# Performance work log

Measured on AMD Instinct MI355X. Metric: run time of the kernel, lower is better.

The kernel has to match this reference:

```python
import jax, jax.numpy as jnp
import numpy as np
import math

B, L, D, P = 2, 2048, 256, 32

def _lin_init(key, fan_in, shape):
    return jax.random.normal(key, shape, dtype=jnp.float32) / np.float32(math.sqrt(fan_in))

def setup_inputs() -> dict:
    key = jax.random.key(0)
    ks = jax.random.split(key, 16)
    return {
        "x": jax.random.normal(ks[0], (B, L, D), dtype=jnp.float32),
        "pos_phases": jax.random.normal(ks[1], (L, P), dtype=jnp.float32) * np.float32(math.pi),
        "w_pos_value": _lin_init(ks[2], D, (D, D)), "b_pos_value": jnp.zeros((D,), jnp.float32),
        "w_key": _lin_init(ks[3], D, (D, P)), "b_key": jnp.zeros((P,), jnp.float32),
        "w_kv": _lin_init(ks[4], D, (D, D)), "b_kv": jnp.zeros((D,), jnp.float32),
        "w_vg1": _lin_init(ks[5], 2 * D, (2 * D, D)), "b_vg1": jnp.zeros((D,), jnp.float32),
        "w_vg2": _lin_init(ks[6], D, (D, 1)), "b_vg2": jnp.zeros((1,), jnp.float32),
        "w_bg1": _lin_init(ks[7], D, (D, D // 2)), "b_bg1": jnp.zeros((D // 2,), jnp.float32),
        "w_bg2": _lin_init(ks[8], D // 2, (D // 2, 2)), "b_bg2": jnp.zeros((2,), jnp.float32),
        "ln_r_g": jnp.ones((D,), jnp.float32), "ln_r_b": jnp.zeros((D,), jnp.float32),
        "w_r1": _lin_init(ks[9], D, (D, 2 * D)), "b_r1": jnp.zeros((2 * D,), jnp.float32),
        "w_r2": _lin_init(ks[10], 2 * D, (2 * D, D)), "b_r2": jnp.zeros((D,), jnp.float32),
        "ln_o_g": jnp.ones((D,), jnp.float32), "ln_o_b": jnp.zeros((D,), jnp.float32),
        "w_out": _lin_init(ks[11], D, (D, D)), "b_out": jnp.zeros((D,), jnp.float32),
    }

def _ln(z, g, b, eps=1e-5):
    mu = z.mean(-1, keepdims=True)
    var = ((z - mu) ** 2).mean(-1, keepdims=True)
    return (z - mu) * jax.lax.rsqrt(var + eps) * g + b

def _shift1(z):
    # torch.roll(shifts=1, dims=1) then zero first position == shift right with zero pad
    return jnp.concatenate([jnp.zeros_like(z[:, :1]), z[:, :-1]], axis=1)

def reference(x, pos_phases, w_pos_value, b_pos_value, w_key, b_key, w_kv, b_kv,
              w_vg1, b_vg1, w_vg2, b_vg2, w_bg1, b_bg1, w_bg2, b_bg2,
              ln_r_g, ln_r_b, w_r1, b_r1, w_r2, b_r2, ln_o_g, ln_o_b, w_out, b_out):
    Bv, Lv, Dv = x.shape
    Pv = pos_phases.shape[1]
    inv_sqrt_p = np.float32(1.0 / math.sqrt(Pv))

    # --- positional memory ---
    pos_phasors = jnp.exp(1j * pos_phases)                      # (L,P) complex64
    pos_values = (x @ w_pos_value + b_pos_value).astype(jnp.complex64)  # (B,L,D)
    pos_bound = pos_phasors[None, :, :, None] * pos_values[:, :, None, :]  # (B,L,P,D)
    pos_memory = jnp.cumsum(pos_bound, axis=1)
    pos_query = jnp.exp(-1j * pos_phases)                       # (L,P)
    pos_retrieved = (pos_memory * pos_query[None, :, :, None]).sum(axis=2).real * inv_sqrt_p

    # --- content-based KV memory ---
    key_phases = jnp.tanh(x @ w_key + b_key) * np.float32(math.pi)  # (B,L,P)
    key_phasors = jnp.exp(1j * key_phases)
    kv_values = (x @ w_kv + b_kv).astype(jnp.complex64)         # (B,L,D)

    x_shifted = _shift1(x)
    gate_input = jnp.concatenate([x, x_shifted], axis=-1)       # (B,L,2D)
    h = jax.nn.gelu(gate_input @ w_vg1 + b_vg1, approximate=False)
    value_gates = jax.nn.sigmoid(h @ w_vg2 + b_vg2)             # (B,L,1)

    key_phasors_shifted = _shift1(key_phasors)                  # (B,L,P)
    kv_bound = (key_phasors_shifted[..., None] * kv_values[:, :, None, :]) \
               * value_gates[:, :, :, None].astype(jnp.complex64)  # (B,L,P,D)
    kv_memory = jnp.cumsum(kv_bound, axis=1)
    gate_cumsum = jnp.maximum(jnp.cumsum(value_gates, axis=1), 1.0)  # (B,L,1)
    kv_query = jnp.exp(-1j * key_phases)                        # (B,L,P)
    kv_retrieved = (kv_memory * kv_query[..., None]).sum(axis=2).real
    kv_retrieved = kv_retrieved / (jnp.sqrt(gate_cumsum) * np.float32(math.sqrt(Pv)))

    # --- blend, refine, output ---
    bg_h = jax.nn.gelu(x @ w_bg1 + b_bg1, approximate=False)
    blend = jax.nn.softmax(bg_h @ w_bg2 + b_bg2, axis=-1)       # (B,L,2)
    blended = blend[..., 0:1] * pos_retrieved + blend[..., 1:2] * kv_retrieved

    refined = jax.nn.gelu(_ln(blended, ln_r_g, ln_r_b) @ w_r1 + b_r1, approximate=False) @ w_r2 + b_r2
    return x + (_ln(refined, ln_o_g, ln_o_b) @ w_out + b_out)
```

## Files before the change

### kernel.cpp

```cpp
#include <hip/hip_runtime.h>
#include <math.h>

#define B_ 2
#define L_ 2048
#define D_ 256
#define P_ 32
#define NC_ 32
#define CL_ 64

#define INV_SQRT_P 0.17677669529663687f
#define PI_F 3.14159265358979323846f

typedef __attribute__((ext_vector_type(8))) short bf16x8;
typedef __attribute__((ext_vector_type(4))) float f32x4;

__device__ __forceinline__ float gelu_exact(float x){
    return 0.5f * x * (1.0f + erff(x * 0.70710678118654752f));
}

__device__ __forceinline__ unsigned short f2bf(float f){
    unsigned int u = __float_as_uint(f);
    u += 0x7FFFu + ((u >> 16) & 1u);
    return (unsigned short)(u >> 16);
}

__device__ __forceinline__ float bf2f(unsigned short u){
    return __uint_as_float(((unsigned int)u) << 16);
}

__global__ __launch_bounds__(256) void k_prep(
    const float* __restrict__ pos_phases,
    const float* __restrict__ w_pv, const float* __restrict__ w_kv,
    const float* __restrict__ w_vg1, const float* __restrict__ w_bg1,
    const float* __restrict__ w_r1, const float* __restrict__ w_r2,
    const float* __restrict__ w_out, const float* __restrict__ w_key,
    unsigned short* __restrict__ wq,
    float* __restrict__ cpos, float* __restrict__ spos)
{
    int id = blockIdx.x * 256 + threadIdx.x;
    if (id < 630784){
        const float* src; int N; int local;
        if (id < 65536)       { src = w_pv;  N = 256; local = id; }
        else if (id < 131072) { src = w_kv;  N = 256; local = id - 65536; }
        else if (id < 262144) { src = w_vg1; N = 256; local = id - 131072; }
        else if (id < 294912) { src = w_bg1; N = 128; local = id - 262144; }
        else if (id < 425984) { src = w_r1;  N = 512; local = id - 294912; }
        else if (id < 557056) { src = w_r2;  N = 256; local = id - 425984; }
        else if (id < 622592) { src = w_out; N = 256; local = id - 557056; }
        else                  { src = w_key; N = 32;  local = id - 622592; }
        int j = local & 7, lane = (local >> 3) & 63, tile = local >> 9;
        int NT = N >> 4;
        int nt = tile % NT, kt = tile / NT;
        int row = kt * 32 + ((lane >> 4) << 3) + j;
        int col = nt * 16 + (lane & 15);
        wq[id] = f2bf(src[(size_t)row * N + col]);
    } else {
        int idx = id - 630784;
        float s, c;
        sincosf(pos_phases[idx], &s, &c);
        cpos[idx] = c;
        spos[idx] = s;
    }
}

__global__ __launch_bounds__(512) void k_proj(
    const float* __restrict__ x,
    const unsigned short* __restrict__ wq,
    const float* __restrict__ b_pv, const float* __restrict__ b_kv,
    const float* __restrict__ b_vg1,
    const float* __restrict__ w_vg2, const float* __restrict__ b_vg2,
    const float* __restrict__ b_bg1,
    const float* __restrict__ w_bg2, const float* __restrict__ b_bg2,
    const float* __restrict__ b_key,
    unsigned short* __restrict__ pvb, unsigned short* __restrict__ kvvb,
    float* __restrict__ ck, float* __restrict__ sk,
    float* __restrict__ vg, float* __restrict__ blend0, float* __restrict__ blend1)
{
    __shared__ float hbuf[16][257];
    __shared__ float kvbuf[16][257];
    __shared__ float bhbuf[16][129];
    __shared__ float kph[16][33];
    __shared__ float red[16][17], red2[16][17], red3[16][17];
    __shared__ float vgs[16];

    const int i = threadIdx.x;
    const int lane = i & 63, w = i >> 6;
    const int b = blockIdx.x >> 7, lt = blockIdx.x & 127, l0 = lt * 16;
    const int g = lane >> 4, c = lane & 15;

    bf16x8 xa[8], xs[8];
    {
        int row  = l0 + (lane & 15);
        int rowp = row - 1;
        const float* xr = x + (size_t)(b * L_ + row) * D_ + ((lane >> 4) << 3);
        #pragma unroll
        for (int kt = 0; kt < 8; ++kt){
            float4 a0 = *(const float4*)(xr + kt * 32);
            float4 a1 = *(const float4*)(xr + kt * 32 + 4);
            bf16x8 v;
            v[0] = (short)f2bf(a0.x); v[1] = (short)f2bf(a0.y);
            v[2] = (short)f2bf(a0.z); v[3] = (short)f2bf(a0.w);
            v[4] = (short)f2bf(a1.x); v[5] = (short)f2bf(a1.y);
            v[6] = (short)f2bf(a1.z); v[7] = (short)f2bf(a1.w);
            xa[kt] = v;
        }
        if (rowp >= 0){
            const float* xp = x + (size_t)(b * L_ + rowp) * D_ + ((lane >> 4) << 3);
            #pragma unroll
            for (int kt = 0; kt < 8; ++kt){
                float4 a0 = *(const float4*)(xp + kt * 32);
                float4 a1 = *(const float4*)(xp + kt * 32 + 4);
                bf16x8 v;
                v[0] = (short)f2bf(a0.x); v[1] = (short)f2bf(a0.y);
                v[2] = (short)f2bf(a0.z); v[3] = (short)f2bf(a0.w);
                v[4] = (short)f2bf(a1.x); v[5] = (short)f2bf(a1.y);
                v[6] = (short)f2bf(a1.z); v[7] = (short)f2bf(a1.w);
                xs[kt] = v;
            }
        } else {
            #pragma unroll
            for (int kt = 0; kt < 8; ++kt){
                bf16x8 v;
                #pragma unroll
                for (int j = 0; j < 8; ++j) v[j] = 0;
                xs[kt] = v;
            }
        }
    }

    const unsigned short* wpv  = wq;
    const unsigned short* wkv  = wq + 65536;
    const unsigned short* wvg1 = wq + 131072;
    const unsigned short* wbg1 = wq + 262144;
    const unsigned short* wkey = wq + 622592;

    for (int jb = w; jb < 58; jb += 8){
        f32x4 acc = {0.f, 0.f, 0.f, 0.f};
        if (jb < 2){
            int nt = jb;
            #pragma unroll
            for (int kt = 0; kt < 8; ++kt){
                bf16x8 bf = *(const bf16x8*)(wkey + (kt * 2 + nt) * 512 + lane * 8);
                acc = __builtin_amdgcn_mfma_f32_16x16x32_bf16(xa[kt], bf, acc, 0, 0, 0);
            }
            float bb = b_key[nt * 16 + c];
            #pragma unroll
            for (int r = 0; r < 4; ++r)
                kph[4 * g + r][nt * 16 + c] = acc[r] + bb;
        } else if (jb < 18){
            int nt = jb - 2;
            #pragma unroll
            for (int kt = 0; kt < 8; ++kt){
                bf16x8 bf = *(const bf16x8*)(wpv + (kt * 16 + nt) * 512 + lane * 8);
                acc = __builtin_amdgcn_mfma_f32_16x16x32_bf16(xa[kt], bf, acc, 0, 0, 0);
            }
            float bb = b_pv[nt * 16 + c];
            #pragma unroll
            for (int r = 0; r < 4; ++r)
                pvb[(size_t)(b * L_ + l0 + 4 * g + r) * D_ + nt * 16 + c] = f2bf(acc[r] + bb);
        } else if (jb < 34){
            int nt = jb - 18;
            #pragma unroll
            for (int kt = 0; kt < 8; ++kt){
                bf16x8 bf = *(const bf16x8*)(wkv + (kt * 16 + nt) * 512 + lane * 8);
                acc = __builtin_amdgcn_mfma_f32_16x16x32_bf16(xa[kt], bf, acc, 0, 0, 0);
            }
            float bb = b_kv[nt * 16 + c];
            #pragma unroll
            for (int r = 0; r < 4; ++r)
                kvbuf[4 * g + r][nt * 16 + c] = acc[r] + bb;
        } else if (jb < 50){
            int nt = jb - 34;
            #pragma unroll
            for (int kt = 0; kt < 8; ++kt){
                bf16x8 bf = *(const bf16x8*)(wvg1 + (kt * 16 + nt) * 512 + lane * 8);
                acc = __builtin_amdgcn_mfma_f32_16x16x32_bf16(xa[kt], bf, acc, 0, 0, 0);
            }
            #pragma unroll
            for (int kt = 8; kt < 16; ++kt){
                bf16x8 bf = *(const bf16x8*)(wvg1 + (kt * 16 + nt) * 512 + lane * 8);
                acc = __builtin_amdgcn_mfma_f32_16x16x32_bf16(xs[kt - 8], bf, acc, 0, 0, 0);
            }
            float bb = b_vg1[nt * 16 + c];
            #pragma unroll
            for (int r = 0; r < 4; ++r)
                hbuf[4 * g + r][nt * 16 + c] = gelu_exact(acc[r] + bb);
        } else {
            int nt = jb - 50;
            #pragma unroll
            for (int kt = 0; kt < 8; ++kt){
                bf16x8 bf = *(const bf16x8*)(wbg1 + (kt * 8 + nt) * 512 + lane * 8);
                acc = __builtin_amdgcn_mfma_f32_16x16x32_bf16(xa[kt], bf, acc, 0, 0, 0);
            }
            float bb = b_bg1[nt * 16 + c];
            #pragma unroll
            for (int r = 0; r < 4; ++r)
                bhbuf[4 * g + r][nt * 16 + c] = gelu_exact(acc[r] + bb);
        }
    }
    __syncthreads();

    {
        int t = i >> 5, p = i & 31;
        float a = tanhf(kph[t][p]) * PI_F;
        float s, cc;
        sincosf(a, &s, &cc);
        ck[(size_t)(b * L_ + l0 + t) * P_ + p] = cc;
        sk[(size_t)(b * L_ + l0 + t) * P_ + p] = s;
    }

    if (i < 256){
        int t = i >> 4, c2 = i & 15;
        float s = 0.f;
        #pragma unroll
        for (int m = 0; m < 16; ++m){ int dd = c2 + 16 * m; s += hbuf[t][dd] * w_vg2[dd]; }
        red[t][c2] = s;
    } else {
        int ii = i - 256;
        int t = ii >> 4, c2 = ii & 15;
        float s0 = 0.f, s1 = 0.f;
        #pragma unroll
        for (int m = 0; m < 8; ++m){
            int jj = c2 + 16 * m;
            float v = bhbuf[t][jj];
            s0 += v * w_bg2[jj * 2 + 0];
            s1 += v * w_bg2[jj * 2 + 1];
        }
        red2[t][c2] = s0; red3[t][c2] = s1;
    }
    __syncthreads();
    if (i < 16){
        float s = 0.f;
        #pragma unroll
        for (int c2 = 0; c2 < 16; ++c2) s += red[i][c2];
        s += b_vg2[0];
        float gv = 1.0f / (1.0f + expf(-s));
        vg[b * L_ + l0 + i] = gv;
        vgs[i] = gv;
    } else if (i < 32){
        int t = i - 16;
        float s0 = 0.f, s1 = 0.f;
        #pragma unroll
        for (int c2 = 0; c2 < 16; ++c2){ s0 += red2[t][c2]; s1 += red3[t][c2]; }
        s0 += b_bg2[0]; s1 += b_bg2[1];
        float mx = fmaxf(s0, s1);
        float e0 = expf(s0 - mx), e1 = expf(s1 - mx);
        float inv = 1.0f / (e0 + e1);
        blend0[b * L_ + l0 + t] = e0 * inv;
        blend1[b * L_ + l0 + t] = e1 * inv;
    }
    __syncthreads();

    {
        int d = i & 255, tg = i >> 8;
        #pragma unroll
        for (int m = 0; m < 8; ++m){
            int tok = tg * 8 + m;
            kvvb[(size_t)(b * L_ + l0 + tok) * D_ + d] = f2bf(kvbuf[tok][d] * vgs[tok]);
        }
    }
}

__global__ __launch_bounds__(256) void k_scan1(
    const float* __restrict__ cpos, const float* __restrict__ spos,
    const float* __restrict__ ck, const float* __restrict__ sk,
    const unsigned short* __restrict__ pvb, const unsigned short* __restrict__ kvvb,
    const float* __restrict__ vg,
    float* __restrict__ posSr, float* __restrict__ posSi,
    float* __restrict__ kvSr, float* __restrict__ kvSi,
    float* __restrict__ rnorm)
{
    const int z = blockIdx.z;
    const int c = blockIdx.x, b = blockIdx.y;
    const int i = threadIdx.x;
    if (z == 8){
        if (c != 0) return;
        float loc[8];
        float run = 0.f;
        #pragma unroll
        for (int m = 0; m < 8; ++m){ run += vg[b * L_ + i * 8 + m]; loc[m] = run; }
        __shared__ float part[256];
        part[i] = run;
        __syncthreads();
        for (int off = 1; off < 256; off <<= 1){
            float t = (i >= off) ? part[i - off] : 0.0f;
            __syncthreads();
            part[i] += t;
            __syncthreads();
        }
        float excl = part[i] - run;
        #pragma unroll
        for (int m = 0; m < 8; ++m){
            float gc = fmaxf(excl + loc[m], 1.0f);
            rnorm[b * L_ + i * 8 + m] = rsqrtf(gc) * INV_SQRT_P;
        }
        return;
    }
    const int type = z >> 2, pg = z & 3;
    const int d = i;
    const int p0 = pg * 8;
    float Sr[8], Si[8];
    #pragma unroll
    for (int j = 0; j < 8; ++j){ Sr[j] = 0.f; Si[j] = 0.f; }

    if (type == 0){
        for (int l = 0; l < CL_; ++l){
            int row = c * CL_ + l;
            float v = bf2f(pvb[(size_t)(b * L_ + row) * D_ + d]);
            float4 c0 = *(const float4*)(cpos + row * P_ + p0);
            float4 c1 = *(const float4*)(cpos + row * P_ + p0 + 4);
            float4 s0 = *(const float4*)(spos + row * P_ + p0);
            float4 s1 = *(const float4*)(spos + row * P_ + p0 + 4);
            Sr[0] = fmaf(c0.x, v, Sr[0]); Si[0] = fmaf(s0.x, v, Si[0]);
            Sr[1] = fmaf(c0.y, v, Sr[1]); Si[1] = fmaf(s0.y, v, Si[1]);
            Sr[2] = fmaf(c0.z, v, Sr[2]); Si[2] = fmaf(s0.z, v, Si[2]);
            Sr[3] = fmaf(c0.w, v, Sr[3]); Si[3] = fmaf(s0.w, v, Si[3]);
            Sr[4] = fmaf(c1.x, v, Sr[4]); Si[4] = fmaf(s1.x, v, Si[4]);
            Sr[5] = fmaf(c1.y, v, Sr[5]); Si[5] = fmaf(s1.y, v, Si[5]);
            Sr[6] = fmaf(c1.z, v, Sr[6]); Si[6] = fmaf(s1.z, v, Si[6]);
            Sr[7] = fmaf(c1.w, v, Sr[7]); Si[7] = fmaf(s1.w, v, Si[7]);
        }
        #pragma unroll
        for (int j = 0; j < 8; ++j){
            size_t o = (size_t)((b * NC_ + c) * P_ + p0 + j) * D_ + d;
            posSr[o] = Sr[j]; posSi[o] = Si[j];
        }
    } else {
        float pc[8], ps[8];
        int srow = c * CL_ - 1;
        if (srow >= 0){
            float4 c0 = *(const float4*)(ck + ((size_t)b * L_ + srow) * P_ + p0);
            float4 c1 = *(const float4*)(ck + ((size_t)b * L_ + srow) * P_ + p0 + 4);
            float4 s0 = *(const float4*)(sk + ((size_t)b * L_ + srow) * P_ + p0);
            float4 s1 = *(const float4*)(sk + ((size_t)b * L_ + srow) * P_ + p0 + 4);
            pc[0]=c0.x; pc[1]=c0.y; pc[2]=c0.z; pc[3]=c0.w;
            pc[4]=c1.x; pc[5]=c1.y; pc[6]=c1.z; pc[7]=c1.w;
            ps[0]=s0.x; ps[1]=s0.y; ps[2]=s0.z; ps[3]=s0.w;
            ps[4]=s1.x; ps[5]=s1.y; ps[6]=s1.z; ps[7]=s1.w;
        } else {
            #pragma unroll
            for (int j = 0; j < 8; ++j){ pc[j] = 0.f; ps[j] = 0.f; }
        }
        for (int l = 0; l < CL_; ++l){
            int row = c * CL_ + l;
            float vv = bf2f(kvvb[(size_t)(b * L_ + row) * D_ + d]);
            float4 c0 = *(const float4*)(ck + ((size_t)b * L_ + row) * P_ + p0);
            float4 c1 = *(const float4*)(ck + ((size_t)b * L_ + row) * P_ + p0 + 4);
            float4 s0 = *(const float4*)(sk + ((size_t)b * L_ + row) * P_ + p0);
            float4 s1 = *(const float4*)(sk + ((size_t)b * L_ + row) * P_ + p0 + 4);
            #pragma unroll
            for (int j = 0; j < 8; ++j){
                Sr[j] = fmaf(pc[j], vv, Sr[j]);
                Si[j] = fmaf(ps[j], vv, Si[j]);
            }
            pc[0]=c0.x; pc[1]=c0.y; pc[2]=c0.z; pc[3]=c0.w;
            pc[4]=c1.x; pc[5]=c1.y; pc[6]=c1.z; pc[7]=c1.w;
            ps[0]=s0.x; ps[1]=s0.y; ps[2]=s0.z; ps[3]=s0.w;
            ps[4]=s1.x; ps[5]=s1.y; ps[6]=s1.z; ps[7]=s1.w;
        }
        #pragma unroll
        for (int j = 0; j < 8; ++j){
            size_t o = (size_t)((b * NC_ + c) * P_ + p0 + j) * D_ + d;
            kvSr[o] = Sr[j]; kvSi[o] = Si[j];
        }
    }
}

__global__ __launch_bounds__(256) void k_prefix(
    float* __restrict__ posSr, float* __restrict__ posSi,
    float* __restrict__ kvSr, float* __restrict__ kvSi)
{
    __shared__ float4 tot_s[64][4];
    const int colLocal = threadIdx.x >> 2, seg = threadIdx.x & 3;
    const int col = blockIdx.x * 64 + colLocal;
    const int a = col >> 12;
    const int rem = col & 4095;
    const int b = rem >> 11;
    const int pd = (rem & 2047) * 4;
    float* A = (a == 0) ? posSr : (a == 1) ? posSi : (a == 2) ? kvSr : kvSi;
    float* base = A + (size_t)b * NC_ * (P_ * D_) + pd;

    float4 t[8];
    #pragma unroll
    for (int k = 0; k < 8; ++k)
        t[k] = *(const float4*)(base + (size_t)(seg * 8 + k) * (P_ * D_));
    float4 tot = {0.f, 0.f, 0.f, 0.f};
    #pragma unroll
    for (int k = 0; k < 8; ++k){
        tot.x += t[k].x; tot.y += t[k].y; tot.z += t[k].z; tot.w += t[k].w;
    }
    tot_s[colLocal][seg] = tot;
    __syncthreads();
    float4 run = {0.f, 0.f, 0.f, 0.f};
    #pragma unroll
    for (int s = 0; s < 3; ++s){
        if (s < seg){
            float4 v = tot_s[colLocal][s];
            run.x += v.x; run.y += v.y; run.z += v.z; run.w += v.w;
        }
    }
    #pragma unroll
    for (int k = 0; k < 8; ++k){
        float4 cur = t[k];
        *(float4*)(base + (size_t)(seg * 8 + k) * (P_ * D_)) = run;
        run.x += cur.x; run.y += cur.y; run.z += cur.z; run.w += cur.w;
    }
}

__global__ __launch_bounds__(256) void k_retrieve(
    const float* __restrict__ cpos, const float* __restrict__ spos,
    const float* __restrict__ ck, const float* __restrict__ sk,
    const unsigned short* __restrict__ pvb, const unsigned short* __restrict__ kvvb,
    const float* __restrict__ rnorm,
    const float* __restrict__ posSr, const float* __restrict__ posSi,
    const float* __restrict__ kvSr, const float* __restrict__ kvSi,
    unsigned short* __restrict__ posretb, unsigned short* __restrict__ kvretb)
{
    const int z = blockIdx.z;
    const int c = blockIdx.x, b = blockIdx.y;
    const int type = z >> 2, dquad = z & 3;
    const int lane = threadIdx.x & 63, wv = threadIdx.x >> 6;
    const int pg = lane >> 4, dl = lane & 15;
    const int d = dquad * 64 + wv * 16 + dl;
    const int p0 = pg * 8;

    float Sr[8], Si[8];

    if (type == 0){
        #pragma unroll
        for (int j = 0; j < 8; ++j){
            size_t o = (size_t)((b * NC_ + c) * P_ + p0 + j) * D_ + d;
            Sr[j] = posSr[o]; Si[j] = posSi[o];
        }
        for (int l = 0; l < CL_; ++l){
            int row = c * CL_ + l;
            float v = bf2f(pvb[(size_t)(b * L_ + row) * D_ + d]);
            float4 c0 = *(const float4*)(cpos + row * P_ + p0);
            float4 c1 = *(const float4*)(cpos + row * P_ + p0 + 4);
            float4 s0 = *(const float4*)(spos + row * P_ + p0);
            float4 s1 = *(const float4*)(spos + row * P_ + p0 + 4);
            float r0 = 0.f, r1 = 0.f, r2 = 0.f, r3 = 0.f;
            Sr[0] = fmaf(c0.x, v, Sr[0]); r0 = fmaf(c0.x, Sr[0], r0);
            Si[0] = fmaf(s0.x, v, Si[0]); r1 = fmaf(s0.x, Si[0], r1);
            Sr[1] = fmaf(c0.y, v, Sr[1]); r2 = fmaf(c0.y, Sr[1], r2);
            Si[1] = fmaf(s0.y, v, Si[1]); r3 = fmaf(s0.y, Si[1], r3);
            Sr[2] = fmaf(c0.z, v, Sr[2]); r0 = fmaf(c0.z, Sr[2], r0);
            Si[2] = fmaf(s0.z, v, Si[2]); r1 = fmaf(s0.z, Si[2], r1);
            Sr[3] = fmaf(c0.w, v, Sr[3]); r2 = fmaf(c0.w, Sr[3], r2);
            Si[3] = fmaf(s0.w, v, Si[3]); r3 = fmaf(s0.w, Si[3], r3);
            Sr[4] = fmaf(c1.x, v, Sr[4]); r0 = fmaf(c1.x, Sr[4], r0);
            Si[4] = fmaf(s1.x, v, Si[4]); r1 = fmaf(s1.x, Si[4], r1);
            Sr[5] = fmaf(c1.y, v, Sr[5]); r2 = fmaf(c1.y, Sr[5], r2);
            Si[5] = fmaf(s1.y, v, Si[5]); r3 = fmaf(s1.y, Si[5], r3);
            Sr[6] = fmaf(c1.z, v, Sr[6]); r0 = fmaf(c1.z, Sr[6], r0);
            Si[6] = fmaf(s1.z, v, Si[6]); r1 = fmaf(s1.z, Si[6], r1);
            Sr[7] = fmaf(c1.w, v, Sr[7]); r2 = fmaf(c1.w, Sr[7], r2);
            Si[7] = fmaf(s1.w, v, Si[7]); r3 = fmaf(s1.w, Si[7], r3);
            float r = (r0 + r1) + (r2 + r3);
            r += __shfl_xor(r, 16, 64);
            r += __shfl_xor(r, 32, 64);
            if (pg == 0)
                posretb[(size_t)(b * L_ + row) * D_ + d] = f2bf(r * INV_SQRT_P);
        }
    } else {
        #pragma unroll
        for (int j = 0; j < 8; ++j){
            size_t o = (size_t)((b * NC_ + c) * P_ + p0 + j) * D_ + d;
            Sr[j] = kvSr[o]; Si[j] = kvSi[o];
        }
        float pc[8], ps[8];
        int srow = c * CL_ - 1;
        if (srow >= 0){
            float4 c0 = *(const float4*)(ck + ((size_t)b * L_ + srow) * P_ + p0);
            float4 c1 = *(const float4*)(ck + ((size_t)b * L_ + srow) * P_ + p0 + 4);
            float4 s0 = *(const float4*)(sk + ((size_t)b * L_ + srow) * P_ + p0);
            float4 s1 = *(const float4*)(sk + ((size_t)b * L_ + srow) * P_ + p0 + 4);
            pc[0]=c0.x; pc[1]=c0.y; pc[2]=c0.z; pc[3]=c0.w;
            pc[4]=c1.x; pc[5]=c1.y; pc[6]=c1.z; pc[7]=c1.w;
            ps[0]=s0.x; ps[1]=s0.y; ps[2]=s0.z; ps[3]=s0.w;
            ps[4]=s1.x; ps[5]=s1.y; ps[6]=s1.z; ps[7]=s1.w;
        } else {
            #pragma unroll
            for (int j = 0; j < 8; ++j){ pc[j] = 0.f; ps[j] = 0.f; }
        }
        for (int l = 0; l < CL_; ++l){
            int row = c * CL_ + l;
            float vv = bf2f(kvvb[(size_t)(b * L_ + row) * D_ + d]);
            float rn = rnorm[b * L_ + row];
            float4 c0 = *(const float4*)(ck + ((size_t)b * L_ + row) * P_ + p0);
            float4 c1 = *(const float4*)(ck + ((size_t)b * L_ + row) * P_ + p0 + 4);
            float4 s0 = *(const float4*)(sk + ((size_t)b * L_ + row) * P_ + p0);
            float4 s1 = *(const float4*)(sk + ((size_t)b * L_ + row) * P_ + p0 + 4);
            float qc[8], qs[8];
            qc[0]=c0.x; qc[1]=c0.y; qc[2]=c0.z; qc[3]=c0.w;
            qc[4]=c1.x; qc[5]=c1.y; qc[6]=c1.z; qc[7]=c1.w;
            qs[0]=s0.x; qs[1]=s0.y; qs[2]=s0.z; qs[3]=s0.w;
            qs[4]=s1.x; qs[5]=s1.y; qs[6]=s1.z; qs[7]=s1.w;
            float r0 = 0.f, r1 = 0.f, r2 = 0.f, r3 = 0.f;
            #pragma unroll
            for (int j = 0; j < 8; ++j){
                Sr[j] = fmaf(pc[j], vv, Sr[j]);
                Si[j] = fmaf(ps[j], vv, Si[j]);
                if (j & 1){ r2 = fmaf(qc[j], Sr[j], r2); r3 = fmaf(qs[j], Si[j], r3); }
                else      { r0 = fmaf(qc[j], Sr[j], r0); r1 = fmaf(qs[j], Si[j], r1); }
                pc[j] = qc[j]; ps[j] = qs[j];
            }
            float r = (r0 + r1) + (r2 + r3);
            r += __shfl_xor(r, 16, 64);
            r += __shfl_xor(r, 32, 64);
            if (pg == 0)
                kvretb[(size_t)(b * L_ + row) * D_ + d] = f2bf(r * rn);
        }
    }
}

__global__ __launch_bounds__(512) void k_final(
    const float* __restrict__ x,
    const unsigned short* __restrict__ posretb, const unsigned short* __restrict__ kvretb,
    const float* __restrict__ blend0, const float* __restrict__ blend1,
    const unsigned short* __restrict__ wq,
    const float* __restrict__ ln_r_g, const float* __restrict__ ln_r_b,
    const float* __restrict__ b_r1, const float* __restrict__ b_r2,
    const float* __restrict__ ln_o_g, const float* __restrict__ ln_o_b,
    const float* __restrict__ b_out,
    float* __restrict__ out)
{
    __shared__ float zbuf[16][257];
    __shared__ __align__(16) unsigned short aA[8][512];
    __shared__ __align__(16) unsigned short aH[16][512];
    __shared__ float red[16][17], red2[16][17];
    __shared__ float mu[16], rs[16];

    const int i = threadIdx.x, lane = i & 63, w = i >> 6;
    const int b = blockIdx.x >> 7, l0 = (blockIdx.x & 127) * 16;
    const int g = lane >> 4, c = lane & 15;
    const unsigned short* wr1  = wq + 294912;
    const unsigned short* wr2  = wq + 425984;
    const unsigned short* wout = wq + 557056;

    {
        int t = i >> 5, c0 = (i & 31) * 8;
        size_t base = (size_t)(b * L_ + l0 + t) * D_ + c0;
        float w0 = blend0[b * L_ + l0 + t], w1 = blend1[b * L_ + l0 + t];
        bf16x8 pp = *(const bf16x8*)(posretb + base);
        bf16x8 kk = *(const bf16x8*)(kvretb + base);
        #pragma unroll
        for (int m = 0; m < 8; ++m)
            zbuf[t][c0 + m] = w0 * bf2f((unsigned short)pp[m])
                            + w1 * bf2f((unsigned short)kk[m]);
    }
    __syncthreads();

    if (i < 256){
        int t = i >> 4, c2 = i & 15;
        float s = 0.f, s2 = 0.f;
        #pragma unroll
        for (int m = 0; m < 16; ++m){ float v = zbuf[t][c2 + 16 * m]; s += v; s2 += v * v; }
        red[t][c2] = s; red2[t][c2] = s2;
    }
    __syncthreads();
    if (i < 16){
        float s = 0.f, s2 = 0.f;
        #pragma unroll
        for (int c2 = 0; c2 < 16; ++c2){ s += red[i][c2]; s2 += red2[i][c2]; }
        float mean = s * (1.0f / 256.0f);
        float var  = s2 * (1.0f / 256.0f) - mean * mean;
        mu[i] = mean; rs[i] = rsqrtf(var + 1e-5f);
    }
    __syncthreads();

    {
        int kt = i >> 6;
        int t2 = lane & 15, kb = kt * 32 + ((lane >> 4) << 3);
        float m_ = mu[t2], r_ = rs[t2];
        bf16x8 v8;
        #pragma unroll
        for (int j = 0; j < 8; ++j){
            int k = kb + j;
            float v = (zbuf[t2][k] - m_) * r_ * ln_r_g[k] + ln_r_b[k];
            v8[j] = (short)f2bf(v);
        }
        *(bf16x8*)&aA[kt][lane * 8] = v8;
    }
    __syncthreads();

    {
        bf16x8 afr[8];
        #pragma unroll
        for (int kt = 0; kt < 8; ++kt) afr[kt] = *(const bf16x8*)&aA[kt][lane * 8];
        for (int q = 0; q < 4; ++q){
            int nt = w + 8 * q;
            f32x4 acc = {0.f, 0.f, 0.f, 0.f};
            #pragma unroll
            for (int kt = 0; kt < 8; ++kt){
                bf16x8 bf = *(const bf16x8*)(wr1 + (kt * 32 + nt) * 512 + lane * 8);
                acc = __builtin_amdgcn_mfma_f32_16x16x32_bf16(afr[kt], bf, acc, 0, 0, 0);
            }
            float bb = b_r1[nt * 16 + c];
            #pragma unroll
            for (int r = 0; r < 4; ++r){
                float hv = gelu_exact(acc[r] + bb);
                int t = 4 * g + r, hcol = nt * 16 + c;
                int kt2 = hcol >> 5, kk = hcol & 31;
                int lane2 = ((kk >> 3) << 4) + t, j2 = kk & 7;
                aH[kt2][lane2 * 8 + j2] = f2bf(hv);
            }
        }
    }
    __syncthreads();

    {
        bf16x8 hfr[16];
        #pragma unroll
        for (int kt = 0; kt < 16; ++kt) hfr[kt] = *(const bf16x8*)&aH[kt][lane * 8];
        for (int q = 0; q < 2; ++q){
            int nt = w + 8 * q;
            f32x4 acc = {0.f, 0.f, 0.f, 0.f};
            #pragma unroll
            for (int kt = 0; kt < 16; ++kt){
                bf16x8 bf = *(const bf16x8*)(wr2 + (kt * 16 + nt) * 512 + lane * 8);
                acc = __builtin_amdgcn_mfma_f32_16x16x32_bf16(hfr[kt], bf, acc, 0, 0, 0);
            }
            float bb = b_r2[nt * 16 + c];
            #pragma unroll
            for (int r = 0; r < 4; ++r)
                zbuf[4 * g + r][nt * 16 + c] = acc[r] + bb;
        }
    }
    __syncthreads();

    if (i < 256){
        int t = i >> 4, c2 = i & 15;
        float s = 0.f, s2 = 0.f;
        #pragma unroll
        for (int m = 0; m < 16; ++m){ float v = zbuf[t][c2 + 16 * m]; s += v; s2 += v * v; }
        red[t][c2] = s; red2[t][c2] = s2;
    }
    __syncthreads();
    if (i < 16){
        float s = 0.f, s2 = 0.f;
        #pragma unroll
        for (int c2 = 0; c2 < 16; ++c2){ s += red[i][c2]; s2 += red2[i][c2]; }
        float mean = s * (1.0f / 256.0f);
        float var  = s2 * (1.0f / 256.0f) - mean * mean;
        mu[i] = mean; rs[i] = rsqrtf(var + 1e-5f);
    }
    __syncthreads();

    {
        int kt = i >> 6;
        int t2 = lane & 15, kb = kt * 32 + ((lane >> 4) << 3);
        float m_ = mu[t2], r_ = rs[t2];
        bf16x8 v8;
        #pragma unroll
        for (int j = 0; j < 8; ++j){
            int k = kb + j;
            float v = (zbuf[t2][k] - m_) * r_ * ln_o_g[k] + ln_o_b[k];
            v8[j] = (short)f2bf(v);
        }
        *(bf16x8*)&aA[kt][lane * 8] = v8;
    }
    __syncthreads();

    {
        bf16x8 azr[8];
        #pragma unroll
        for (int kt = 0; kt < 8; ++kt) azr[kt] = *(const bf16x8*)&aA[kt][lane * 8];
        for (int q = 0; q < 2; ++q){
            int nt = w + 8 * q;
            f32x4 acc = {0.f, 0.f, 0.f, 0.f};
            #pragma unroll
            for (int kt = 0; kt < 8; ++kt){
                bf16x8 bf = *(const bf16x8*)(wout + (kt * 16 + nt) * 512 + lane * 8);
                acc = __builtin_amdgcn_mfma_f32_16x16x32_bf16(azr[kt], bf, acc, 0, 0, 0);
            }
            float bb = b_out[nt * 16 + c];
            #pragma unroll
            for (int r = 0; r < 4; ++r){
                size_t o = (size_t)(b * L_ + l0 + 4 * g + r) * D_ + nt * 16 + c;
                out[o] = x[o] + acc[r] + bb;
            }
        }
    }
}

extern "C" void kernel_launch(void* const* d_in, const int* in_sizes, int n_in,
                              void* d_out, int out_size, void* d_ws, size_t ws_size,
                              hipStream_t stream) {
    const float* x          = (const float*)d_in[0];
    const float* pos_phases = (const float*)d_in[1];
    const float* w_pv       = (const float*)d_in[2];
    const float* b_pv       = (const float*)d_in[3];
    const float* w_key      = (const float*)d_in[4];
    const float* b_key      = (const float*)d_in[5];
    const float* w_kv       = (const float*)d_in[6];
    const float* b_kv       = (const float*)d_in[7];
    const float* w_vg1      = (const float*)d_in[8];
    const float* b_vg1      = (const float*)d_in[9];
    const float* w_vg2      = (const float*)d_in[10];
    const float* b_vg2      = (const float*)d_in[11];
    const float* w_bg1      = (const float*)d_in[12];
    const float* b_bg1      = (const float*)d_in[13];
    const float* w_bg2      = (const float*)d_in[14];
    const float* b_bg2      = (const float*)d_in[15];
    const float* ln_r_g     = (const float*)d_in[16];
    const float* ln_r_b     = (const float*)d_in[17];
    const float* w_r1       = (const float*)d_in[18];
    const float* b_r1       = (const float*)d_in[19];
    const float* w_r2       = (const float*)d_in[20];
    const float* b_r2       = (const float*)d_in[21];
    const float* ln_o_g     = (const float*)d_in[22];
    const float* ln_o_b     = (const float*)d_in[23];
    const float* w_out      = (const float*)d_in[24];
    const float* b_out      = (const float*)d_in[25];
    float* out = (float*)d_out;

    float* ws = (float*)d_ws;
    size_t off = 0;
    float* cpos   = ws + off; off += (size_t)L_ * P_;
    float* spos   = ws + off; off += (size_t)L_ * P_;
    float* ck     = ws + off; off += (size_t)B_ * L_ * P_;
    float* sk     = ws + off; off += (size_t)B_ * L_ * P_;
    float* vg     = ws + off; off += (size_t)B_ * L_;
    float* rnorm  = ws + off; off += (size_t)B_ * L_;
    float* blend0 = ws + off; off += (size_t)B_ * L_;
    float* blend1 = ws + off; off += (size_t)B_ * L_;
    float* posSr  = ws + off; off += (size_t)B_ * NC_ * P_ * D_;
    float* posSi  = ws + off; off += (size_t)B_ * NC_ * P_ * D_;
    float* kvSr   = ws + off; off += (size_t)B_ * NC_ * P_ * D_;
    float* kvSi   = ws + off; off += (size_t)B_ * NC_ * P_ * D_;
    unsigned short* wq      = (unsigned short*)(ws + off); off += 630784 / 2;
    unsigned short* pvb     = (unsigned short*)(ws + off); off += (size_t)B_ * L_ * D_ / 2;
    unsigned short* kvvb    = (unsigned short*)(ws + off); off += (size_t)B_ * L_ * D_ / 2;
    unsigned short* posretb = (unsigned short*)(ws + off); off += (size_t)B_ * L_ * D_ / 2;
    unsigned short* kvretb  = (unsigned short*)(ws + off); off += (size_t)B_ * L_ * D_ / 2;

    k_prep<<<2720, 256, 0, stream>>>(pos_phases,
        w_pv, w_kv, w_vg1, w_bg1, w_r1, w_r2, w_out, w_key,
        wq, cpos, spos);

    k_proj<<<B_ * 128, 512, 0, stream>>>(x, wq,
        b_pv, b_kv, b_vg1, w_vg2, b_vg2, b_bg1, w_bg2, b_bg2, b_key,
        pvb, kvvb, ck, sk, vg, blend0, blend1);

    k_scan1<<<dim3(NC_, B_, 9), 256, 0, stream>>>(cpos, spos, ck, sk, pvb, kvvb, vg,
                                                  posSr, posSi, kvSr, kvSi, rnorm);

    k_prefix<<<256, 256, 0, stream>>>(posSr, posSi, kvSr, kvSi);

    k_retrieve<<<dim3(NC_, B_, 8), 256, 0, stream>>>(cpos, spos, ck, sk, pvb, kvvb,
                                                     rnorm,
                                                     posSr, posSi, kvSr, kvSi,
                                                     posretb, kvretb);

    k_final<<<B_ * 128, 512, 0, stream>>>(x, posretb, kvretb, blend0, blend1, wq,
        ln_r_g, ln_r_b, b_r1, b_r2, ln_o_g, ln_o_b, b_out, out);
}
```

Measured before the change: 103.5 us.

## Halve scan chunk length and process 32 rows per block in final MLP

Doubles the number of scan chunks (chunk length 64→32), raising parallelism in the chunked scan and retrieve kernels, and extends the prefix kernel to 8 segments per column. The final kernel now handles 32 rows per block, so each weight fragment loaded from global memory feeds two MFMA row tiles. The r1/r2 GEMMs are split into two halves to fit the hidden buffer in LDS. LDS intermediates are stored as bf16, which saves LDS space but adds rounding before the layer norms; the final kernel also launches half as many blocks.

```diff
diff --git a/kernel.cpp b/kernel.cpp
--- a/kernel.cpp
+++ b/kernel.cpp
@@ -5,8 +5,8 @@
 #define L_ 2048
 #define D_ 256
 #define P_ 32
-#define NC_ 32
-#define CL_ 64
+#define NC_ 64
+#define CL_ 32
 
 #define INV_SQRT_P 0.17677669529663687f
 #define PI_F 3.14159265358979323846f
@@ -370,9 +370,9 @@
     float* __restrict__ posSr, float* __restrict__ posSi,
     float* __restrict__ kvSr, float* __restrict__ kvSi)
 {
-    __shared__ float4 tot_s[64][4];
-    const int colLocal = threadIdx.x >> 2, seg = threadIdx.x & 3;
-    const int col = blockIdx.x * 64 + colLocal;
+    __shared__ float4 tot_s[32][8];
+    const int colLocal = threadIdx.x >> 3, seg = threadIdx.x & 7;
+    const int col = blockIdx.x * 32 + colLocal;
     const int a = col >> 12;
     const int rem = col & 4095;
     const int b = rem >> 11;
@@ -393,7 +393,7 @@
     __syncthreads();
     float4 run = {0.f, 0.f, 0.f, 0.f};
     #pragma unroll
-    for (int s = 0; s < 3; ++s){
+    for (int s = 0; s < 7; ++s){
         if (s < seg){
             float4 v = tot_s[colLocal][s];
             run.x += v.x; run.y += v.y; run.z += v.z; run.w += v.w;
@@ -525,44 +525,47 @@
     const float* __restrict__ b_out,
     float* __restrict__ out)
 {
-    __shared__ float zbuf[16][257];
-    __shared__ __align__(16) unsigned short aA[8][512];
-    __shared__ __align__(16) unsigned short aH[16][512];
-    __shared__ float red[16][17], red2[16][17];
-    __shared__ float mu[16], rs[16];
+    __shared__ unsigned short zb[32][264];
+    __shared__ __align__(16) unsigned short aA[8][1024];
+    __shared__ __align__(16) unsigned short aH[8][1024];
+    __shared__ float mu[32], rs[32];
+    float* redb = (float*)&aA[0][0];
 
     const int i = threadIdx.x, lane = i & 63, w = i >> 6;
-    const int b = blockIdx.x >> 7, l0 = (blockIdx.x & 127) * 16;
+    const int b = blockIdx.x >> 6, l0 = (blockIdx.x & 63) * 32;
     const int g = lane >> 4, c = lane & 15;
     const unsigned short* wr1  = wq + 294912;
     const unsigned short* wr2  = wq + 425984;
     const unsigned short* wout = wq + 557056;
 
     {
-        int t = i >> 5, c0 = (i & 31) * 8;
+        int t = i >> 4, c0 = (i & 15) * 16;
         size_t base = (size_t)(b * L_ + l0 + t) * D_ + c0;
         float w0 = blend0[b * L_ + l0 + t], w1 = blend1[b * L_ + l0 + t];
-        bf16x8 pp = *(const bf16x8*)(posretb + base);
-        bf16x8 kk = *(const bf16x8*)(kvretb + base);
-        #pragma unroll
-        for (int m = 0; m < 8; ++m)
-            zbuf[t][c0 + m] = w0 * bf2f((unsigned short)pp[m])
-                            + w1 * bf2f((unsigned short)kk[m]);
-    }
-    __syncthreads();
-
-    if (i < 256){
+        #pragma unroll
+        for (int h = 0; h < 2; ++h){
+            bf16x8 pp = *(const bf16x8*)(posretb + base + 8 * h);
+            bf16x8 kk = *(const bf16x8*)(kvretb + base + 8 * h);
+            #pragma unroll
+            for (int m = 0; m < 8; ++m)
+                zb[t][c0 + 8 * h + m] = f2bf(w0 * bf2f((unsigned short)pp[m])
+                                           + w1 * bf2f((unsigned short)kk[m]));
+        }
+    }
+    __syncthreads();
+
+    {
         int t = i >> 4, c2 = i & 15;
         float s = 0.f, s2 = 0.f;
         #pragma unroll
-        for (int m = 0; m < 16; ++m){ float v = zbuf[t][c2 + 16 * m]; s += v; s2 += v * v; }
-        red[t][c2] = s; red2[t][c2] = s2;
-    }
-    __syncthreads();
-    if (i < 16){
+        for (int m = 0; m < 16; ++m){ float v = bf2f(zb[t][c2 + 16 * m]); s += v; s2 += v * v; }
+        redb[t * 17 + c2] = s; redb[544 + t * 17 + c2] = s2;
+    }
+    __syncthreads();
+    if (i < 32){
         float s = 0.f, s2 = 0.f;
         #pragma unroll
-        for (int c2 = 0; c2 < 16; ++c2){ s += red[i][c2]; s2 += red2[i][c2]; }
+        for (int c2 = 0; c2 < 16; ++c2){ s += redb[i * 17 + c2]; s2 += redb[544 + i * 17 + c2]; }
         float mean = s * (1.0f / 256.0f);
         float var  = s2 * (1.0f / 256.0f) - mean * mean;
         mu[i] = mean; rs[i] = rsqrtf(var + 1e-5f);
@@ -571,76 +574,107 @@
 
     {
         int kt = i >> 6;
-        int t2 = lane & 15, kb = kt * 32 + ((lane >> 4) << 3);
-        float m_ = mu[t2], r_ = rs[t2];
-        bf16x8 v8;
-        #pragma unroll
-        for (int j = 0; j < 8; ++j){
-            int k = kb + j;
-            float v = (zbuf[t2][k] - m_) * r_ * ln_r_g[k] + ln_r_b[k];
-            v8[j] = (short)f2bf(v);
-        }
-        *(bf16x8*)&aA[kt][lane * 8] = v8;
-    }
-    __syncthreads();
-
-    {
-        bf16x8 afr[8];
-        #pragma unroll
-        for (int kt = 0; kt < 8; ++kt) afr[kt] = *(const bf16x8*)&aA[kt][lane * 8];
-        for (int q = 0; q < 4; ++q){
-            int nt = w + 8 * q;
-            f32x4 acc = {0.f, 0.f, 0.f, 0.f};
-            #pragma unroll
-            for (int kt = 0; kt < 8; ++kt){
-                bf16x8 bf = *(const bf16x8*)(wr1 + (kt * 32 + nt) * 512 + lane * 8);
-                acc = __builtin_amdgcn_mfma_f32_16x16x32_bf16(afr[kt], bf, acc, 0, 0, 0);
-            }
+        int kb = kt * 32 + ((lane >> 4) << 3);
+        #pragma unroll
+        for (int rt = 0; rt < 2; ++rt){
+            int t2 = rt * 16 + (lane & 15);
+            float m_ = mu[t2], r_ = rs[t2];
+            bf16x8 v8;
+            #pragma unroll
+            for (int j = 0; j < 8; ++j){
+                int k = kb + j;
+                float v = (bf2f(zb[t2][k]) - m_) * r_ * ln_r_g[k] + ln_r_b[k];
+                v8[j] = (short)f2bf(v);
+            }
+            *(bf16x8*)&aA[kt][rt * 512 + lane * 8] = v8;
+        }
+    }
+    __syncthreads();
+
+    f32x4 accR2[2][2];
+    #pragma unroll
+    for (int q = 0; q < 2; ++q)
+        #pragma unroll
+        for (int rt = 0; rt < 2; ++rt)
+            accR2[q][rt] = (f32x4){0.f, 0.f, 0.f, 0.f};
+
+    for (int half = 0; half < 2; ++half){
+        #pragma unroll
+        for (int q = 0; q < 2; ++q){
+            int ntl = w + 8 * q;
+            int nt = half * 16 + ntl;
+            bf16x8 bf[8];
+            #pragma unroll
+            for (int kt = 0; kt < 8; ++kt)
+                bf[kt] = *(const bf16x8*)(wr1 + (kt * 32 + nt) * 512 + lane * 8);
             float bb = b_r1[nt * 16 + c];
             #pragma unroll
-            for (int r = 0; r < 4; ++r){
-                float hv = gelu_exact(acc[r] + bb);
-                int t = 4 * g + r, hcol = nt * 16 + c;
-                int kt2 = hcol >> 5, kk = hcol & 31;
-                int lane2 = ((kk >> 3) << 4) + t, j2 = kk & 7;
-                aH[kt2][lane2 * 8 + j2] = f2bf(hv);
-            }
-        }
-    }
-    __syncthreads();
-
-    {
-        bf16x8 hfr[16];
-        #pragma unroll
-        for (int kt = 0; kt < 16; ++kt) hfr[kt] = *(const bf16x8*)&aH[kt][lane * 8];
+            for (int rt = 0; rt < 2; ++rt){
+                f32x4 acc = {0.f, 0.f, 0.f, 0.f};
+                #pragma unroll
+                for (int kt = 0; kt < 8; ++kt){
+                    bf16x8 afr = *(const bf16x8*)&aA[kt][rt * 512 + lane * 8];
+                    acc = __builtin_amdgcn_mfma_f32_16x16x32_bf16(afr, bf[kt], acc, 0, 0, 0);
+                }
+                #pragma unroll
+                for (int r = 0; r < 4; ++r){
+                    float hv = gelu_exact(acc[r] + bb);
+                    int t_tile = 4 * g + r;
+                    int hcol = ntl * 16 + c;
+                    int kt2 = hcol >> 5, kk = hcol & 31;
+                    int lane2 = ((kk >> 3) << 4) + t_tile, j2 = kk & 7;
+                    aH[kt2][rt * 512 + lane2 * 8 + j2] = f2bf(hv);
+                }
+            }
+        }
+        __syncthreads();
+        #pragma unroll
         for (int q = 0; q < 2; ++q){
-            int nt = w + 8 * q;
-            f32x4 acc = {0.f, 0.f, 0.f, 0.f};
-            #pragma unroll
-            for (int kt = 0; kt < 16; ++kt){
-                bf16x8 bf = *(const bf16x8*)(wr2 + (kt * 16 + nt) * 512 + lane * 8);
-                acc = __builtin_amdgcn_mfma_f32_16x16x32_bf16(hfr[kt], bf, acc, 0, 0, 0);
-            }
-            float bb = b_r2[nt * 16 + c];
-            #pragma unroll
-            for (int r = 0; r < 4; ++r)
-                zbuf[4 * g + r][nt * 16 + c] = acc[r] + bb;
-        }
-    }
-    __syncthreads();
-
-    if (i < 256){
+            int nt2 = w + 8 * q;
+            bf16x8 bf2[8];
+            #pragma unroll
+            for (int ktl = 0; ktl < 8; ++ktl)
+                bf2[ktl] = *(const bf16x8*)(wr2 + ((half * 8 + ktl) * 16 + nt2) * 512 + lane * 8);
+            #pragma unroll
+            for (int rt = 0; rt < 2; ++rt){
+                f32x4 acc = accR2[q][rt];
+                #pragma unroll
+                for (int ktl = 0; ktl < 8; ++ktl){
+                    bf16x8 hfr = *(const bf16x8*)&aH[ktl][rt * 512 + lane * 8];
+                    acc = __builtin_amdgcn_mfma_f32_16x16x32_bf16(hfr, bf2[ktl], acc, 0, 0, 0);
+                }
+                accR2[q][rt] = acc;
+            }
+        }
+        __syncthreads();
+    }
+
+    {
+        #pragma unroll
+        for (int q = 0; q < 2; ++q){
+            int nt2 = w + 8 * q;
+            float bb = b_r2[nt2 * 16 + c];
+            #pragma unroll
+            for (int rt = 0; rt < 2; ++rt)
+                #pragma unroll
+                for (int r = 0; r < 4; ++r)
+                    zb[rt * 16 + 4 * g + r][nt2 * 16 + c] = f2bf(accR2[q][rt][r] + bb);
+        }
+    }
+    __syncthreads();
+
+    {
         int t = i >> 4, c2 = i & 15;
         float s = 0.f, s2 = 0.f;
         #pragma unroll
-        for (int m = 0; m < 16; ++m){ float v = zbuf[t][c2 + 16 * m]; s += v; s2 += v * v; }
-        red[t][c2] = s; red2[t][c2] = s2;
-    }
-    __syncthreads();
-    if (i < 16){
+        for (int m = 0; m < 16; ++m){ float v = bf2f(zb[t][c2 + 16 * m]); s += v; s2 += v * v; }
+        redb[t * 17 + c2] = s; redb[544 + t * 17 + c2] = s2;
+    }
+    __syncthreads();
+    if (i < 32){
         float s = 0.f, s2 = 0.f;
         #pragma unroll
-        for (int c2 = 0; c2 < 16; ++c2){ s += red[i][c2]; s2 += red2[i][c2]; }
+        for (int c2 = 0; c2 < 16; ++c2){ s += redb[i * 17 + c2]; s2 += redb[544 + i * 17 + c2]; }
         float mean = s * (1.0f / 256.0f);
         float var  = s2 * (1.0f / 256.0f) - mean * mean;
         mu[i] = mean; rs[i] = rsqrtf(var + 1e-5f);
@@ -649,36 +683,45 @@
 
     {
         int kt = i >> 6;
-        int t2 = lane & 15, kb = kt * 32 + ((lane >> 4) << 3);
-        float m_ = mu[t2], r_ = rs[t2];
-        bf16x8 v8;
-        #pragma unroll
-        for (int j = 0; j < 8; ++j){
-            int k = kb + j;
-            float v = (zbuf[t2][k] - m_) * r_ * ln_o_g[k] + ln_o_b[k];
-            v8[j] = (short)f2bf(v);
-        }
-        *(bf16x8*)&aA[kt][lane * 8] = v8;
-    }
-    __syncthreads();
-
-    {
-        bf16x8 azr[8];
-        #pragma unroll
-        for (int kt = 0; kt < 8; ++kt) azr[kt] = *(const bf16x8*)&aA[kt][lane * 8];
+        int kb = kt * 32 + ((lane >> 4) << 3);
+        #pragma unroll
+        for (int rt = 0; rt < 2; ++rt){
+            int t2 = rt * 16 + (lane & 15);
+            float m_ = mu[t2], r_ = rs[t2];
+            bf16x8 v8;
+            #pragma unroll
+            for (int j = 0; j < 8; ++j){
+                int k = kb + j;
+                float v = (bf2f(zb[t2][k]) - m_) * r_ * ln_o_g[k] + ln_o_b[k];
+                v8[j] = (short)f2bf(v);
+            }
+            *(bf16x8*)&aA[kt][rt * 512 + lane * 8] = v8;
+        }
+    }
+    __syncthreads();
+
+    {
+        #pragma unroll
         for (int q = 0; q < 2; ++q){
             int nt = w + 8 * q;
-            f32x4 acc = {0.f, 0.f, 0.f, 0.f};
-            #pragma unroll
-            for (int kt = 0; kt < 8; ++kt){
-                bf16x8 bf = *(const bf16x8*)(wout + (kt * 16 + nt) * 512 + lane * 8);
-                acc = __builtin_amdgcn_mfma_f32_16x16x32_bf16(azr[kt], bf, acc, 0, 0, 0);
-            }
+            bf16x8 bfo[8];
+            #pragma unroll
+            for (int kt = 0; kt < 8; ++kt)
+                bfo[kt] = *(const bf16x8*)(wout + (kt * 16 + nt) * 512 + lane * 8);
             float bb = b_out[nt * 16 + c];
             #pragma unroll
-            for (int r = 0; r < 4; ++r){
-                size_t o = (size_t)(b * L_ + l0 + 4 * g + r) * D_ + nt * 16 + c;
-                out[o] = x[o] + acc[r] + bb;
+            for (int rt = 0; rt < 2; ++rt){
+                f32x4 acc = {0.f, 0.f, 0.f, 0.f};
+                #pragma unroll
+                for (int kt = 0; kt < 8; ++kt){
+                    bf16x8 azr = *(const bf16x8*)&aA[kt][rt * 512 + lane * 8];
+                    acc = __builtin_amdgcn_mfma_f32_16x16x32_bf16(azr, bfo[kt], acc, 0, 0, 0);
+                }
+                #pragma unroll
+                for (int r = 0; r < 4; ++r){
+                    size_t o = (size_t)(b * L_ + l0 + rt * 16 + 4 * g + r) * D_ + nt * 16 + c;
+                    out[o] = x[o] + acc[r] + bb;
+                }
             }
         }
     }
@@ -746,13 +789,13 @@
     k_scan1<<<dim3(NC_, B_, 9), 256, 0, stream>>>(cpos, spos, ck, sk, pvb, kvvb, vg,
                                                   posSr, posSi, kvSr, kvSi, rnorm);
 
-    k_prefix<<<256, 256, 0, stream>>>(posSr, posSi, kvSr, kvSi);
+    k_prefix<<<512, 256, 0, stream>>>(posSr, posSi, kvSr, kvSi);
 
     k_retrieve<<<dim3(NC_, B_, 8), 256, 0, stream>>>(cpos, spos, ck, sk, pvb, kvvb,
                                                      rnorm,
                                                      posSr, posSi, kvSr, kvSi,
                                                      posretb, kvretb);
 
-    k_final<<<B_ * 128, 512, 0, stream>>>(x, posretb, kvretb, blend0, blend1, wq,
+    k_final<<<B_ * 64, 512, 0, stream>>>(x, posretb, kvretb, blend0, blend1, wq,
         ln_r_g, ln_r_b, b_r1, b_r2, ln_o_g, ln_o_b, b_out, out);
 }
```

Result: faster. 90.28 us (-12.7%).
